# Performance work log

Hardware: AMD Instinct MI355X
Metric: run time of the kernel (lower is better)

## Reference

```python
import jax, jax.numpy as jnp
import numpy as np

N_NODES = 100000
N_EDGES = 500000
N_REL = 6
IN_DIM = 64
HID = 128
HEADS = 4
C = HID // HEADS  # 32 per-head channels
N_GRAPHS = 1024
EPS = 1e-16


def setup_inputs() -> dict:
    key = jax.random.key(0)
    ks = jax.random.split(key, 20)
    x = jax.random.normal(ks[0], (N_NODES, IN_DIM), dtype=jnp.float32)
    edge_index = jax.random.randint(ks[1], (N_REL, 2, N_EDGES), 0, N_NODES, dtype=jnp.int64)
    batch = jnp.sort(jax.random.randint(ks[2], (N_NODES,), 0, N_GRAPHS, dtype=jnp.int64))
    s = 0.02
    return {
        "x": x, "edge_index": edge_index, "batch": batch,
        # layer1 GAT params (stacked over 6 relations)
        "W1": jax.random.normal(ks[3], (N_REL, IN_DIM, HID), dtype=jnp.float32) * s,
        "as1": jax.random.normal(ks[4], (N_REL, HEADS, C), dtype=jnp.float32) * s,
        "ad1": jax.random.normal(ks[5], (N_REL, HEADS, C), dtype=jnp.float32) * s,
        "b1": jnp.zeros((N_REL, HID), dtype=jnp.float32),
        # layer2 GAT params
        "W2": jax.random.normal(ks[6], (N_REL, HID, HID), dtype=jnp.float32) * s,
        "as2": jax.random.normal(ks[7], (N_REL, HEADS, C), dtype=jnp.float32) * s,
        "ad2": jax.random.normal(ks[8], (N_REL, HEADS, C), dtype=jnp.float32) * s,
        "b2": jnp.zeros((N_REL, HID), dtype=jnp.float32),
        # layernorms
        "g1": jnp.ones((HID,), dtype=jnp.float32), "be1": jnp.zeros((HID,), dtype=jnp.float32),
        "g2": jnp.ones((HID,), dtype=jnp.float32), "be2": jnp.zeros((HID,), dtype=jnp.float32),
        # attention pooling query + output proj
        "q": jax.random.normal(ks[9], (HID,), dtype=jnp.float32) * s,
        "Wp": jax.random.normal(ks[10], (HID, HID), dtype=jnp.float32) * s,
        "bp": jnp.zeros((HID,), dtype=jnp.float32),
    }


def _gat_hetero_layer(x, edge_index, W, a_src, a_dst, b):
    # HeteroConv(aggr='sum') over R GATConv relations, add_self_loops=False, eval (no dropout)
    N = x.shape[0]
    out = jnp.zeros((N, HEADS * C), dtype=x.dtype)
    for r in range(N_REL):
        h = (x @ W[r]).reshape(N, HEADS, C)          # [N,H,C]
        al_s = (h * a_src[r]).sum(-1)                # [N,H]
        al_d = (h * a_dst[r]).sum(-1)                # [N,H]
        src, dst = edge_index[r, 0], edge_index[r, 1]
        e = jax.nn.leaky_relu(al_s[src] + al_d[dst], 0.2)   # [E,H]
        m = jax.ops.segment_max(e, dst, num_segments=N)
        ex = jnp.exp(e - m[dst])
        den = jax.ops.segment_sum(ex, dst, num_segments=N)
        alpha = ex / (den[dst] + EPS)                # segment softmax over incoming edges
        msg = h[src] * alpha[:, :, None]             # [E,H,C]
        agg = jax.ops.segment_sum(msg, dst, num_segments=N).reshape(N, HEADS * C)
        out = out + agg + b[r]
    return out


def _layernorm(x, g, b):
    mu = x.mean(-1, keepdims=True)
    v = ((x - mu) ** 2).mean(-1, keepdims=True)
    return (x - mu) * jax.lax.rsqrt(v + 1e-5) * g + b


def _softsign(x):
    return x / (1.0 + jnp.abs(x))


def reference(x, edge_index, batch, W1, as1, ad1, b1, W2, as2, ad2, b2,
              g1, be1, g2, be2, q, Wp, bp):
    h = _gat_hetero_layer(x, edge_index, W1, as1, ad1, b1)
    h = _layernorm(_softsign(h), g1, be1)
    h = _gat_hetero_layer(h, edge_index, W2, as2, ad2, b2)
    h = _layernorm(_softsign(h), g2, be2)
    # attention pooling: segment softmax over batch, then weighted scatter-sum
    scores = (h * q).sum(-1)                                   # [N]
    m = jax.ops.segment_max(scores, batch, num_segments=N_GRAPHS)
    ex = jnp.exp(scores - m[batch])
    den = jax.ops.segment_sum(ex, batch, num_segments=N_GRAPHS)
    w = ex / (den[batch] + EPS)
    pooled = jax.ops.segment_sum(h * w[:, None], batch, num_segments=N_GRAPHS)  # [G,HID]
    return pooled @ Wp + bp
```

## Files before the change

### kernel.cpp

```cpp
#include <hip/hip_runtime.h>
#include <hip/hip_bf16.h>
#include <hip/hip_fp16.h>

#define N_NODES_C 100000
#define N_EDGES_C 500000
#define N_REL_C 6
#define IN_DIM_C 64
#define HID_C 128
#define HEADS_C 4
#define CPH_C 32
#define N_GRAPHS_C 1024
#define NBLK_SCAN 391

typedef _Float16 f16x8 __attribute__((ext_vector_type(8)));
typedef float f32x4 __attribute__((ext_vector_type(4)));

__global__ __launch_bounds__(256) void hist_rank_kernel(const int* __restrict__ ei,
                                                        int* __restrict__ cnt,
                                                        int* __restrict__ rank) {
    int i = blockIdx.x * 256 + threadIdx.x;
    if (i >= N_REL_C * N_EDGES_C) return;
    int r = i / N_EDGES_C;
    int e = i - r * N_EDGES_C;
    int dst = ei[(size_t)r * 2 * N_EDGES_C + N_EDGES_C + e];
    rank[i] = atomicAdd(&cnt[r * N_NODES_C + dst], 1);
}

__global__ __launch_bounds__(256) void scan1_kernel(const int* __restrict__ cnt,
                                                    int* __restrict__ rowptr,
                                                    int* __restrict__ blocksums) {
    int r = blockIdx.y, b = blockIdx.x, t = threadIdx.x;
    int idx = b * 256 + t;
    int v = (idx < N_NODES_C) ? cnt[r * N_NODES_C + idx] : 0;
    int orig = v;
    int lane = t & 63, w = t >> 6;
#pragma unroll
    for (int off = 1; off < 64; off <<= 1) {
        int n = __shfl_up(v, off);
        if (lane >= off) v += n;
    }
    __shared__ int wt[4];
    if (lane == 63) wt[w] = v;
    __syncthreads();
    int add = 0;
    for (int i = 0; i < w; i++) add += wt[i];
    v += add;
    if (idx < N_NODES_C) rowptr[(size_t)r * (N_NODES_C + 1) + idx] = v - orig;
    if (t == 255) blocksums[r * NBLK_SCAN + b] = v;
}

__global__ __launch_bounds__(512) void scan2_kernel(int* __restrict__ blocksums) {
    int r = blockIdx.x, t = threadIdx.x;
    int v = (t < NBLK_SCAN) ? blocksums[r * NBLK_SCAN + t] : 0;
    int orig = v;
    int lane = t & 63, w = t >> 6;
#pragma unroll
    for (int off = 1; off < 64; off <<= 1) {
        int n = __shfl_up(v, off);
        if (lane >= off) v += n;
    }
    __shared__ int wt[8];
    if (lane == 63) wt[w] = v;
    __syncthreads();
    int add = 0;
    for (int i = 0; i < w; i++) add += wt[i];
    v += add;
    if (t < NBLK_SCAN) blocksums[r * NBLK_SCAN + t] = v - orig;
}

__global__ __launch_bounds__(256) void scan3_kernel(int* __restrict__ rowptr,
                                                    const int* __restrict__ blocksums) {
    int r = blockIdx.y, b = blockIdx.x, t = threadIdx.x;
    int idx = b * 256 + t;
    if (idx < N_NODES_C) {
        rowptr[(size_t)r * (N_NODES_C + 1) + idx] += blocksums[r * NBLK_SCAN + b];
    }
    if (b == 0 && t == 0) rowptr[(size_t)r * (N_NODES_C + 1) + N_NODES_C] = N_EDGES_C;
}

__global__ __launch_bounds__(256) void scatter_kernel(const int* __restrict__ ei,
                                                      const int* __restrict__ rowptr,
                                                      const int* __restrict__ rank,
                                                      int* __restrict__ srcids) {
    int i = blockIdx.x * 256 + threadIdx.x;
    if (i >= N_REL_C * N_EDGES_C) return;
    int r = i / N_EDGES_C;
    int e = i - r * N_EDGES_C;
    int src = ei[(size_t)r * 2 * N_EDGES_C + e];
    int dst = ei[(size_t)r * 2 * N_EDGES_C + N_EDGES_C + e];
    int pos = rowptr[(size_t)r * (N_NODES_C + 1) + dst] + rank[i];
    srcids[(size_t)r * N_EDGES_C + pos] = src;
}

__global__ __launch_bounds__(256) void convert_x_kernel(const float* __restrict__ x,
                                                        __half* __restrict__ xh, int n4) {
    int i = blockIdx.x * 256 + threadIdx.x;
    if (i >= n4) return;
    float4 v = ((const float4*)x)[i];
    union { __half h[4]; uint2 u; } u;
    u.h[0] = __float2half(v.x); u.h[1] = __float2half(v.y);
    u.h[2] = __float2half(v.z); u.h[3] = __float2half(v.w);
    ((uint2*)xh)[i] = u.u;
}

__global__ __launch_bounds__(256) void convert_w_kernel(const float* __restrict__ W1,
                                                        const float* __restrict__ W2,
                                                        __half* __restrict__ Wt1,
                                                        __half* __restrict__ Wt2) {
    int i = blockIdx.x * 256 + threadIdx.x;
    if (i < N_REL_C * IN_DIM_C * HID_C) {
        int r = i / (IN_DIM_C * HID_C);
        int rem = i - r * (IN_DIM_C * HID_C);
        int k = rem / HID_C, n = rem - k * HID_C;
        Wt1[(size_t)r * HID_C * IN_DIM_C + n * IN_DIM_C + k] = __float2half(W1[i]);
    }
    if (i < N_REL_C * HID_C * HID_C) {
        int r = i / (HID_C * HID_C);
        int rem = i - r * (HID_C * HID_C);
        int k = rem / HID_C, n = rem - k * HID_C;
        Wt2[(size_t)r * HID_C * HID_C + n * HID_C + k] = __float2half(W2[i]);
    }
}

template <int K>
__global__ __launch_bounds__(256) void gemm_mfma_kernel(
    const __half* __restrict__ Xh, const __half* __restrict__ Wtbase,
    __half* __restrict__ Hbase,
    const float* __restrict__ asbase, const float* __restrict__ adbase,
    float* __restrict__ alsbase, float* __restrict__ aldbase) {
    const int slot = blockIdx.y;
    const __half* Wt = Wtbase + (size_t)slot * HID_C * K;
    __half* H = Hbase + (size_t)slot * N_NODES_C * HID_C;
    const int wave = threadIdx.x >> 6, lane = threadIdx.x & 63;
    const int r0 = blockIdx.x * 64 + wave * 16;
    const int m = lane & 15, quad = lane >> 4;
    int arow = r0 + m;
    if (arow > N_NODES_C - 1) arow = N_NODES_C - 1;
    const __half* ap = Xh + (size_t)arow * K + quad * 8;
    const __half* bp = Wt + (size_t)m * K + quad * 8;

    f32x4 acc[8];
#pragma unroll
    for (int t = 0; t < 8; t++) acc[t] = (f32x4){0.f, 0.f, 0.f, 0.f};

#pragma unroll
    for (int kc = 0; kc < K; kc += 32) {
        f16x8 a = *(const f16x8*)(ap + kc);
#pragma unroll
        for (int t = 0; t < 8; t++) {
            f16x8 b = *(const f16x8*)(bp + (size_t)t * 16 * K + kc);
            acc[t] = __builtin_amdgcn_mfma_f32_16x16x32_f16(a, b, acc[t], 0, 0, 0);
        }
    }

#pragma unroll
    for (int i = 0; i < 4; i++) {
        int R = r0 + quad * 4 + i;
        if (R < N_NODES_C) {
            __half* hp = H + (size_t)R * HID_C + m;
#pragma unroll
            for (int t = 0; t < 8; t++) hp[t * 16] = __float2half(acc[t][i]);
        }
    }

    const float* a_s = asbase + slot * HID_C;
    const float* a_d = adbase + slot * HID_C;
    float* als = alsbase + (size_t)slot * N_NODES_C * HEADS_C;
    float* ald = aldbase + (size_t)slot * N_NODES_C * HEADS_C;
    float ps[4][4], pd[4][4];
#pragma unroll
    for (int h = 0; h < 4; h++) {
        float as0 = a_s[h * 32 + m], as1 = a_s[h * 32 + 16 + m];
        float ad0 = a_d[h * 32 + m], ad1 = a_d[h * 32 + 16 + m];
#pragma unroll
        for (int i = 0; i < 4; i++) {
            ps[h][i] = acc[2 * h][i] * as0 + acc[2 * h + 1][i] * as1;
            pd[h][i] = acc[2 * h][i] * ad0 + acc[2 * h + 1][i] * ad1;
        }
    }
#pragma unroll
    for (int off = 1; off < 16; off <<= 1) {
#pragma unroll
        for (int h = 0; h < 4; h++)
#pragma unroll
            for (int i = 0; i < 4; i++) {
                ps[h][i] += __shfl_xor(ps[h][i], off);
                pd[h][i] += __shfl_xor(pd[h][i], off);
            }
    }
#pragma unroll
    for (int h = 0; h < 4; h++) {
        if (m == h) {
#pragma unroll
            for (int i = 0; i < 4; i++) {
                int R = r0 + quad * 4 + i;
                if (R < N_NODES_C) {
                    als[R * HEADS_C + h] = ps[h][i];
                    ald[R * HEADS_C + h] = pd[h][i];
                }
            }
        }
    }
}

__global__ __launch_bounds__(256) void csr_agg_kernel(
    const int* __restrict__ rowptr, const int* __restrict__ srcids,
    const __half* __restrict__ A, const float* __restrict__ als,
    const float* __restrict__ ald, int rel_start, int rel_cnt,
    const float* __restrict__ bias, int first, int last,
    float* __restrict__ B,
    const float* __restrict__ g, const float* __restrict__ be,
    __half* __restrict__ Cbh) {
    int node = blockIdx.x * 4 + (threadIdx.x >> 6);
    int lane = threadIdx.x & 63;
    int grp = lane >> 4;
    int j16 = lane & 15;
    int head = j16 >> 2;
    int cbase = j16 * 8;

    float acc[8];
    if (first) {
#pragma unroll
        for (int t = 0; t < 8; t++) {
            float s = 0.f;
#pragma unroll
            for (int r = 0; r < N_REL_C; r++) s += bias[r * HID_C + cbase + t];
            acc[t] = s;
        }
    } else {
        float4 b0 = *(const float4*)(B + (size_t)node * HID_C + cbase);
        float4 b1 = *(const float4*)(B + (size_t)node * HID_C + cbase + 4);
        acc[0] = b0.x; acc[1] = b0.y; acc[2] = b0.z; acc[3] = b0.w;
        acc[4] = b1.x; acc[5] = b1.y; acc[6] = b1.z; acc[7] = b1.w;
    }

    for (int j = 0; j < rel_cnt; j++) {
        int r = rel_start + j;
        const int* rp = rowptr + (size_t)r * (N_NODES_C + 1);
        const int* sp = srcids + (size_t)r * N_EDGES_C;
        const __half* Aj = A + (size_t)j * N_NODES_C * HID_C;
        const float* alj = als + (size_t)j * N_NODES_C * HEADS_C;
        float aldv = ald[(size_t)j * N_NODES_C * HEADS_C + node * HEADS_C + head];
        int s = rp[node], e = rp[node + 1];
        float racc[8];
#pragma unroll
        for (int t = 0; t < 8; t++) racc[t] = 0.f;
        float rden = 0.f;

        union HU { uint4 u; _Float16 h[8]; };
        int i = s + grp;
        int src = (i < e) ? sp[i] : 0;
        HU rw; rw.u = *(const uint4*)(Aj + (size_t)src * HID_C + cbase);
        float lg = alj[src * HEADS_C + head];
        for (; i < e; i += 4) {
            int nsrc = (i + 4 < e) ? sp[i + 4] : 0;
            HU nrw; nrw.u = *(const uint4*)(Aj + (size_t)nsrc * HID_C + cbase);
            float nlg = alj[nsrc * HEADS_C + head];
            float v = lg + aldv;
            v = fmaxf(v, 0.2f * v);
            float ex = __expf(v);
            rden += ex;
#pragma unroll
            for (int t = 0; t < 8; t++)
                racc[t] = fmaf((float)rw.h[t], ex, racc[t]);
            src = nsrc; rw = nrw; lg = nlg;
        }
#pragma unroll
        for (int off = 16; off < 64; off <<= 1) {
            rden += __shfl_xor(rden, off);
#pragma unroll
            for (int t = 0; t < 8; t++) racc[t] += __shfl_xor(racc[t], off);
        }
        float inv = 1.f / (rden + 1e-16f);
#pragma unroll
        for (int t = 0; t < 8; t++) acc[t] = fmaf(racc[t], inv, acc[t]);
    }

    if (!last) {
        if (grp == 0) {
            float4 o0 = make_float4(acc[0], acc[1], acc[2], acc[3]);
            float4 o1 = make_float4(acc[4], acc[5], acc[6], acc[7]);
            *(float4*)(B + (size_t)node * HID_C + cbase) = o0;
            *(float4*)(B + (size_t)node * HID_C + cbase + 4) = o1;
        }
    } else {
        float ss[8];
        float sum = 0.f, sq = 0.f;
#pragma unroll
        for (int t = 0; t < 8; t++) {
            float v = acc[t] / (1.f + fabsf(acc[t]));
            ss[t] = v;
            sum += v;
            sq = fmaf(v, v, sq);
        }
#pragma unroll
        for (int off = 1; off < 16; off <<= 1) {
            sum += __shfl_xor(sum, off);
            sq += __shfl_xor(sq, off);
        }
        float mu = sum * (1.f / 128.f);
        float var = sq * (1.f / 128.f) - mu * mu;
        float inv = rsqrtf(var + 1e-5f);
        if (grp == 0) {
            float4 gv0 = *(const float4*)(g + cbase);
            float4 gv1 = *(const float4*)(g + cbase + 4);
            float4 bv0 = *(const float4*)(be + cbase);
            float4 bv1 = *(const float4*)(be + cbase + 4);
            union { uint4 u; __half2 h2[4]; } ow;
            ow.h2[0] = __float22half2_rn(make_float2(
                (ss[0] - mu) * inv * gv0.x + bv0.x, (ss[1] - mu) * inv * gv0.y + bv0.y));
            ow.h2[1] = __float22half2_rn(make_float2(
                (ss[2] - mu) * inv * gv0.z + bv0.z, (ss[3] - mu) * inv * gv0.w + bv0.w));
            ow.h2[2] = __float22half2_rn(make_float2(
                (ss[4] - mu) * inv * gv1.x + bv1.x, (ss[5] - mu) * inv * gv1.y + bv1.y));
            ow.h2[3] = __float22half2_rn(make_float2(
                (ss[6] - mu) * inv * gv1.z + bv1.z, (ss[7] - mu) * inv * gv1.w + bv1.w));
            *(uint4*)(Cbh + (size_t)node * HID_C + cbase) = ow.u;
        }
    }
}

__device__ __forceinline__ int lower_bound_i(const int* __restrict__ a, int n, int v) {
    int lo = 0, hi = n;
    while (lo < hi) {
        int mid = (lo + hi) >> 1;
        if (a[mid] < v) lo = mid + 1; else hi = mid;
    }
    return lo;
}

__global__ void pool_kernel(const __half* __restrict__ H, const int* __restrict__ batch,
                            const float* __restrict__ q, float* __restrict__ pooled) {
    int g = blockIdx.x;
    int lane = threadIdx.x;
    int start = lower_bound_i(batch, N_NODES_C, g);
    int end = lower_bound_i(batch, N_NODES_C, g + 1);
    float q0 = q[lane * 2], q1 = q[lane * 2 + 1];
    float p0 = 0.f, p1 = 0.f, den = 0.f;
    for (int n = start; n < end; n++) {
        float2 hv = __half22float2(*(const __half2*)(H + (size_t)n * HID_C + lane * 2));
        float part = hv.x * q0 + hv.y * q1;
#pragma unroll
        for (int off = 1; off < 64; off <<= 1) part += __shfl_xor(part, off);
        float exs = __expf(part);
        den += exs;
        p0 = fmaf(exs, hv.x, p0);
        p1 = fmaf(exs, hv.y, p1);
    }
    float w = 1.f / (den + 1e-16f);
    pooled[(size_t)g * HID_C + lane * 2] = p0 * w;
    pooled[(size_t)g * HID_C + lane * 2 + 1] = p1 * w;
}

__global__ __launch_bounds__(128) void proj_kernel(const float* __restrict__ pooled,
                                                   const float* __restrict__ Wp,
                                                   const float* __restrict__ bp,
                                                   float* __restrict__ out) {
    int g = blockIdx.x, c = threadIdx.x;
    __shared__ float pl[HID_C];
    pl[c] = pooled[(size_t)g * HID_C + c];
    __syncthreads();
    float s = bp[c];
    for (int k = 0; k < HID_C; k++) s = fmaf(pl[k], Wp[k * HID_C + c], s);
    out[(size_t)g * HID_C + c] = s;
}

extern "C" void kernel_launch(void* const* d_in, const int* in_sizes, int n_in,
                              void* d_out, int out_size, void* d_ws, size_t ws_size,
                              hipStream_t stream) {
    const float* x   = (const float*)d_in[0];
    const int* ei    = (const int*)d_in[1];
    const int* batch = (const int*)d_in[2];
    const float* W1  = (const float*)d_in[3];
    const float* as1 = (const float*)d_in[4];
    const float* ad1 = (const float*)d_in[5];
    const float* b1  = (const float*)d_in[6];
    const float* W2  = (const float*)d_in[7];
    const float* as2 = (const float*)d_in[8];
    const float* ad2 = (const float*)d_in[9];
    const float* b2  = (const float*)d_in[10];
    const float* g1  = (const float*)d_in[11];
    const float* be1 = (const float*)d_in[12];
    const float* g2  = (const float*)d_in[13];
    const float* be2 = (const float*)d_in[14];
    const float* q   = (const float*)d_in[15];
    const float* Wp  = (const float*)d_in[16];
    const float* bp  = (const float*)d_in[17];
    float* out = (float*)d_out;

    const size_t NH = (size_t)N_NODES_C * HID_C;
    char* w = (char*)d_ws;
    __half* xh    = (__half*)w;   w += (size_t)N_NODES_C * IN_DIM_C * 2;
    __half* Cbh   = (__half*)w;   w += NH * 2;
    __half* Wt1   = (__half*)w;   w += (size_t)N_REL_C * IN_DIM_C * HID_C * 2;
    __half* Wt2   = (__half*)w;   w += (size_t)N_REL_C * HID_C * HID_C * 2;
    float* pooled = (float*)w;    w += (size_t)N_GRAPHS_C * HID_C * 4;
    int* rowptr   = (int*)w;      w += ((size_t)N_REL_C * (N_NODES_C + 1) * 4 + 15) & ~15ull;
    int* srcids   = (int*)w;      w += (size_t)N_REL_C * N_EDGES_C * 4;
    int* cnt      = (int*)w;      w += (size_t)N_REL_C * N_NODES_C * 4;
    int* bsums    = (int*)w;      w += ((size_t)N_REL_C * NBLK_SCAN * 4 + 15) & ~15ull;

    const size_t fixed_bytes = (size_t)(w - (char*)d_ws);
    const size_t slot_bytes = NH * 2 + 2 * (size_t)N_NODES_C * HEADS_C * 4;
    int nA = 1;
    float* B = nullptr;
    {
        size_t rem = (ws_size > fixed_bytes) ? (ws_size - fixed_bytes) : 0;
        size_t k = rem / slot_bytes;
        if (k >= 6) {
            nA = 6;
        } else {
            size_t rem2 = (rem > NH * 4) ? (rem - NH * 4) : 0;
            size_t k2 = rem2 / slot_bytes;
            nA = (int)(k2 < 1 ? 1 : (k2 > 5 ? 5 : k2));
        }
    }
    float* als = (float*)w;
    float* ald = als + (size_t)nA * N_NODES_C * HEADS_C;
    __half* A  = (__half*)(ald + (size_t)nA * N_NODES_C * HEADS_C);
    if (nA < 6) B = (float*)(A + (size_t)nA * NH);
    int* rank = (int*)A;

    hipMemsetAsync(cnt, 0, (size_t)N_REL_C * N_NODES_C * sizeof(int), stream);
    const int ehg = (N_REL_C * N_EDGES_C + 255) / 256;
    hist_rank_kernel<<<ehg, 256, 0, stream>>>(ei, cnt, rank);
    scan1_kernel<<<dim3(NBLK_SCAN, N_REL_C), 256, 0, stream>>>(cnt, rowptr, bsums);
    scan2_kernel<<<N_REL_C, 512, 0, stream>>>(bsums);
    scan3_kernel<<<dim3(NBLK_SCAN, N_REL_C), 256, 0, stream>>>(rowptr, bsums);
    scatter_kernel<<<ehg, 256, 0, stream>>>(ei, rowptr, rank, srcids);

    convert_x_kernel<<<(N_NODES_C * IN_DIM_C / 4 + 255) / 256, 256, 0, stream>>>(
        x, xh, N_NODES_C * IN_DIM_C / 4);
    convert_w_kernel<<<(N_REL_C * HID_C * HID_C + 255) / 256, 256, 0, stream>>>(
        W1, W2, Wt1, Wt2);

    const int gemm_grid = (N_NODES_C + 63) / 64;
    const int agg_grid = N_NODES_C / 4;

    for (int gs = 0; gs < N_REL_C; gs += nA) {
        int c2 = (N_REL_C - gs) < nA ? (N_REL_C - gs) : nA;
        gemm_mfma_kernel<IN_DIM_C><<<dim3(gemm_grid, c2), 256, 0, stream>>>(
            xh, Wt1 + (size_t)gs * IN_DIM_C * HID_C, A,
            as1 + gs * HID_C, ad1 + gs * HID_C, als, ald);
        csr_agg_kernel<<<agg_grid, 256, 0, stream>>>(
            rowptr, srcids, A, als, ald, gs, c2,
            b1, (gs == 0) ? 1 : 0, (gs + c2 == N_REL_C) ? 1 : 0,
            B, g1, be1, Cbh);
    }
    for (int gs = 0; gs < N_REL_C; gs += nA) {
        int c2 = (N_REL_C - gs) < nA ? (N_REL_C - gs) : nA;
        gemm_mfma_kernel<HID_C><<<dim3(gemm_grid, c2), 256, 0, stream>>>(
            Cbh, Wt2 + (size_t)gs * HID_C * HID_C, A,
            as2 + gs * HID_C, ad2 + gs * HID_C, als, ald);
        csr_agg_kernel<<<agg_grid, 256, 0, stream>>>(
            rowptr, srcids, A, als, ald, gs, c2,
            b2, (gs == 0) ? 1 : 0, (gs + c2 == N_REL_C) ? 1 : 0,
            B, g2, be2, Cbh);
    }

    pool_kernel<<<N_GRAPHS_C, 64, 0, stream>>>(Cbh, batch, q, pooled);
    proj_kernel<<<N_GRAPHS_C, 128, 0, stream>>>(pooled, Wp, bp, out);
}
```

Measured before the change: 1.113 ms.

## Slice CSR scatter, merge converts, deepen agg prefetch, parallelize pooling across waves

The CSR scatter now runs as 8 output-address slices, so each block only writes srcids positions inside its slice and the random writes become more localized. This costs reading every edge 8 times. The x and W fp16 conversions are merged into one launch. The aggregation kernel prefetches two edges ahead and defers the cross-group accumulator shuffles to once per node instead of once per relation. Pooling uses 4 waves per graph with a shared-memory reduction instead of a single serial wave.

Measured after the change: 1.175 ms. 5.6% more time.

```diff
diff --git a/kernel.cpp b/kernel.cpp
--- a/kernel.cpp
+++ b/kernel.cpp
@@ -11,6 +11,8 @@
 #define CPH_C 32
 #define N_GRAPHS_C 1024
 #define NBLK_SCAN 391
+#define SC_CHUNK 16384
+#define SC_NCHUNK 184
 
 typedef _Float16 f16x8 __attribute__((ext_vector_type(8)));
 typedef float f32x4 __attribute__((ext_vector_type(4)));
@@ -78,36 +80,43 @@
     if (b == 0 && t == 0) rowptr[(size_t)r * (N_NODES_C + 1) + N_NODES_C] = N_EDGES_C;
 }
 
-__global__ __launch_bounds__(256) void scatter_kernel(const int* __restrict__ ei,
-                                                      const int* __restrict__ rowptr,
-                                                      const int* __restrict__ rank,
-                                                      int* __restrict__ srcids) {
+__global__ __launch_bounds__(256) void scatter_sliced_kernel(const int* __restrict__ ei,
+                                                             const int* __restrict__ rowptr,
+                                                             const int* __restrict__ rank,
+                                                             int* __restrict__ srcids) {
+    const int total = N_REL_C * N_EDGES_C;
+    int bid = blockIdx.x;
+    int slice = bid & 7;
+    int chunk = bid >> 3;
+    int lo = slice * (total / 8);
+    int hi = lo + total / 8;
+    int base = chunk * SC_CHUNK;
+    int end = base + SC_CHUNK;
+    if (end > total) end = total;
+    for (int i = base + threadIdx.x; i < end; i += 256) {
+        int r = i / N_EDGES_C;
+        int e = i - r * N_EDGES_C;
+        int src = ei[(size_t)r * 2 * N_EDGES_C + e];
+        int dst = ei[(size_t)r * 2 * N_EDGES_C + N_EDGES_C + e];
+        int pos = r * N_EDGES_C + rowptr[(size_t)r * (N_NODES_C + 1) + dst] + rank[i];
+        if (pos >= lo && pos < hi) srcids[pos] = src;
+    }
+}
+
+__global__ __launch_bounds__(256) void convert_all_kernel(const float* __restrict__ x,
+                                                          __half* __restrict__ xh,
+                                                          const float* __restrict__ W1,
+                                                          const float* __restrict__ W2,
+                                                          __half* __restrict__ Wt1,
+                                                          __half* __restrict__ Wt2) {
     int i = blockIdx.x * 256 + threadIdx.x;
-    if (i >= N_REL_C * N_EDGES_C) return;
-    int r = i / N_EDGES_C;
-    int e = i - r * N_EDGES_C;
-    int src = ei[(size_t)r * 2 * N_EDGES_C + e];
-    int dst = ei[(size_t)r * 2 * N_EDGES_C + N_EDGES_C + e];
-    int pos = rowptr[(size_t)r * (N_NODES_C + 1) + dst] + rank[i];
-    srcids[(size_t)r * N_EDGES_C + pos] = src;
-}
-
-__global__ __launch_bounds__(256) void convert_x_kernel(const float* __restrict__ x,
-                                                        __half* __restrict__ xh, int n4) {
-    int i = blockIdx.x * 256 + threadIdx.x;
-    if (i >= n4) return;
-    float4 v = ((const float4*)x)[i];
-    union { __half h[4]; uint2 u; } u;
-    u.h[0] = __float2half(v.x); u.h[1] = __float2half(v.y);
-    u.h[2] = __float2half(v.z); u.h[3] = __float2half(v.w);
-    ((uint2*)xh)[i] = u.u;
-}
-
-__global__ __launch_bounds__(256) void convert_w_kernel(const float* __restrict__ W1,
-                                                        const float* __restrict__ W2,
-                                                        __half* __restrict__ Wt1,
-                                                        __half* __restrict__ Wt2) {
-    int i = blockIdx.x * 256 + threadIdx.x;
+    if (i < N_NODES_C * IN_DIM_C / 4) {
+        float4 v = ((const float4*)x)[i];
+        union { __half h[4]; uint2 u; } u;
+        u.h[0] = __float2half(v.x); u.h[1] = __float2half(v.y);
+        u.h[2] = __float2half(v.z); u.h[3] = __float2half(v.w);
+        ((uint2*)xh)[i] = u.u;
+    }
     if (i < N_REL_C * IN_DIM_C * HID_C) {
         int r = i / (IN_DIM_C * HID_C);
         int rem = i - r * (IN_DIM_C * HID_C);
@@ -219,21 +228,10 @@
     int cbase = j16 * 8;
 
     float acc[8];
-    if (first) {
-#pragma unroll
-        for (int t = 0; t < 8; t++) {
-            float s = 0.f;
-#pragma unroll
-            for (int r = 0; r < N_REL_C; r++) s += bias[r * HID_C + cbase + t];
-            acc[t] = s;
-        }
-    } else {
-        float4 b0 = *(const float4*)(B + (size_t)node * HID_C + cbase);
-        float4 b1 = *(const float4*)(B + (size_t)node * HID_C + cbase + 4);
-        acc[0] = b0.x; acc[1] = b0.y; acc[2] = b0.z; acc[3] = b0.w;
-        acc[4] = b1.x; acc[5] = b1.y; acc[6] = b1.z; acc[7] = b1.w;
-    }
-
+#pragma unroll
+    for (int t = 0; t < 8; t++) acc[t] = 0.f;
+
+    union HU { uint4 u; _Float16 h[8]; };
     for (int j = 0; j < rel_cnt; j++) {
         int r = rel_start + j;
         const int* rp = rowptr + (size_t)r * (N_NODES_C + 1);
@@ -247,33 +245,52 @@
         for (int t = 0; t < 8; t++) racc[t] = 0.f;
         float rden = 0.f;
 
-        union HU { uint4 u; _Float16 h[8]; };
         int i = s + grp;
-        int src = (i < e) ? sp[i] : 0;
-        HU rw; rw.u = *(const uint4*)(Aj + (size_t)src * HID_C + cbase);
-        float lg = alj[src * HEADS_C + head];
+        int srcA = (i < e) ? sp[i] : 0;
+        int srcB = (i + 4 < e) ? sp[i + 4] : 0;
+        HU rwA; rwA.u = *(const uint4*)(Aj + (size_t)srcA * HID_C + cbase);
+        float lgA = alj[srcA * HEADS_C + head];
+        HU rwB; rwB.u = *(const uint4*)(Aj + (size_t)srcB * HID_C + cbase);
+        float lgB = alj[srcB * HEADS_C + head];
         for (; i < e; i += 4) {
-            int nsrc = (i + 4 < e) ? sp[i + 4] : 0;
-            HU nrw; nrw.u = *(const uint4*)(Aj + (size_t)nsrc * HID_C + cbase);
-            float nlg = alj[nsrc * HEADS_C + head];
-            float v = lg + aldv;
+            int srcC = (i + 8 < e) ? sp[i + 8] : 0;
+            HU rwC; rwC.u = *(const uint4*)(Aj + (size_t)srcC * HID_C + cbase);
+            float lgC = alj[srcC * HEADS_C + head];
+            float v = lgA + aldv;
             v = fmaxf(v, 0.2f * v);
             float ex = __expf(v);
             rden += ex;
 #pragma unroll
             for (int t = 0; t < 8; t++)
-                racc[t] = fmaf((float)rw.h[t], ex, racc[t]);
-            src = nsrc; rw = nrw; lg = nlg;
-        }
-#pragma unroll
-        for (int off = 16; off < 64; off <<= 1) {
-            rden += __shfl_xor(rden, off);
-#pragma unroll
-            for (int t = 0; t < 8; t++) racc[t] += __shfl_xor(racc[t], off);
-        }
+                racc[t] = fmaf((float)rwA.h[t], ex, racc[t]);
+            rwA = rwB; lgA = lgB;
+            rwB = rwC; lgB = lgC;
+        }
+        rden += __shfl_xor(rden, 16);
+        rden += __shfl_xor(rden, 32);
         float inv = 1.f / (rden + 1e-16f);
 #pragma unroll
         for (int t = 0; t < 8; t++) acc[t] = fmaf(racc[t], inv, acc[t]);
+    }
+
+#pragma unroll
+    for (int off = 16; off < 64; off <<= 1)
+#pragma unroll
+        for (int t = 0; t < 8; t++) acc[t] += __shfl_xor(acc[t], off);
+
+    if (first) {
+#pragma unroll
+        for (int t = 0; t < 8; t++) {
+            float s = 0.f;
+#pragma unroll
+            for (int r = 0; r < N_REL_C; r++) s += bias[r * HID_C + cbase + t];
+            acc[t] += s;
+        }
+    } else {
+        float4 b0 = *(const float4*)(B + (size_t)node * HID_C + cbase);
+        float4 b1 = *(const float4*)(B + (size_t)node * HID_C + cbase + 4);
+        acc[0] += b0.x; acc[1] += b0.y; acc[2] += b0.z; acc[3] += b0.w;
+        acc[4] += b1.x; acc[5] += b1.y; acc[6] += b1.z; acc[7] += b1.w;
     }
 
     if (!last) {
@@ -329,15 +346,18 @@
     return lo;
 }
 
-__global__ void pool_kernel(const __half* __restrict__ H, const int* __restrict__ batch,
-                            const float* __restrict__ q, float* __restrict__ pooled) {
+__global__ __launch_bounds__(256) void pool_kernel(const __half* __restrict__ H,
+                                                   const int* __restrict__ batch,
+                                                   const float* __restrict__ q,
+                                                   float* __restrict__ pooled) {
     int g = blockIdx.x;
-    int lane = threadIdx.x;
+    int t = threadIdx.x;
+    int wave = t >> 6, lane = t & 63;
     int start = lower_bound_i(batch, N_NODES_C, g);
     int end = lower_bound_i(batch, N_NODES_C, g + 1);
     float q0 = q[lane * 2], q1 = q[lane * 2 + 1];
     float p0 = 0.f, p1 = 0.f, den = 0.f;
-    for (int n = start; n < end; n++) {
+    for (int n = start + wave; n < end; n += 4) {
         float2 hv = __half22float2(*(const __half2*)(H + (size_t)n * HID_C + lane * 2));
         float part = hv.x * q0 + hv.y * q1;
 #pragma unroll
@@ -347,9 +367,20 @@
         p0 = fmaf(exs, hv.x, p0);
         p1 = fmaf(exs, hv.y, p1);
     }
-    float w = 1.f / (den + 1e-16f);
-    pooled[(size_t)g * HID_C + lane * 2] = p0 * w;
-    pooled[(size_t)g * HID_C + lane * 2 + 1] = p1 * w;
+    __shared__ float sp[4][HID_C];
+    __shared__ float sden[4];
+    sp[wave][lane * 2] = p0;
+    sp[wave][lane * 2 + 1] = p1;
+    if (lane == 0) sden[wave] = den;
+    __syncthreads();
+    if (wave == 0) {
+        float a0 = sp[0][lane * 2] + sp[1][lane * 2] + sp[2][lane * 2] + sp[3][lane * 2];
+        float a1 = sp[0][lane * 2 + 1] + sp[1][lane * 2 + 1] + sp[2][lane * 2 + 1] + sp[3][lane * 2 + 1];
+        float d = sden[0] + sden[1] + sden[2] + sden[3];
+        float w = 1.f / (d + 1e-16f);
+        pooled[(size_t)g * HID_C + lane * 2] = a0 * w;
+        pooled[(size_t)g * HID_C + lane * 2 + 1] = a1 * w;
+    }
 }
 
 __global__ __launch_bounds__(128) void proj_kernel(const float* __restrict__ pooled,
@@ -427,12 +458,10 @@
     scan1_kernel<<<dim3(NBLK_SCAN, N_REL_C), 256, 0, stream>>>(cnt, rowptr, bsums);
     scan2_kernel<<<N_REL_C, 512, 0, stream>>>(bsums);
     scan3_kernel<<<dim3(NBLK_SCAN, N_REL_C), 256, 0, stream>>>(rowptr, bsums);
-    scatter_kernel<<<ehg, 256, 0, stream>>>(ei, rowptr, rank, srcids);
-
-    convert_x_kernel<<<(N_NODES_C * IN_DIM_C / 4 + 255) / 256, 256, 0, stream>>>(
-        x, xh, N_NODES_C * IN_DIM_C / 4);
-    convert_w_kernel<<<(N_REL_C * HID_C * HID_C + 255) / 256, 256, 0, stream>>>(
-        W1, W2, Wt1, Wt2);
+    scatter_sliced_kernel<<<SC_NCHUNK * 8, 256, 0, stream>>>(ei, rowptr, rank, srcids);
+
+    convert_all_kernel<<<(N_NODES_C * IN_DIM_C / 4 + 255) / 256, 256, 0, stream>>>(
+        x, xh, W1, W2, Wt1, Wt2);
 
     const int gemm_grid = (N_NODES_C + 63) / 64;
     const int agg_grid = N_NODES_C / 4;
@@ -458,6 +487,6 @@
             B, g2, be2, Cbh);
     }
 
-    pool_kernel<<<N_GRAPHS_C, 64, 0, stream>>>(Cbh, batch, q, pooled);
+    pool_kernel<<<N_GRAPHS_C, 256, 0, stream>>>(Cbh, batch, q, pooled);
     proj_kernel<<<N_GRAPHS_C, 128, 0, stream>>>(pooled, Wp, bp, out);
 }
```
